# Kernel optimization log

Hardware: AMD Instinct MI355X
Metric: run time of the kernel (lower is better)

Reference implementation:

```python
import jax, jax.numpy as jnp
import numpy as np

RES = 128          # image / k-space resolution
DECIMATION = 4     # acceleration factor
P = RES * RES // DECIMATION  # 4096 trajectory points
B = 8              # batch


def setup_inputs() -> dict:
    key = jax.random.key(0)
    k1, k2 = jax.random.split(key)
    k_space_input = jax.random.normal(k1, (B, 1, RES, RES, 2), dtype=jnp.float32)
    # learnable k-space trajectory in pixel units, range [-RES/2, RES/2]
    trajectory = (jax.random.uniform(k2, (P, 2), dtype=jnp.float32) - 0.5) * RES
    return {"k_space_input": k_space_input, "trajectory": trajectory}


def _grid_sample_points(img, pts_norm):
    """torch.nn.functional.grid_sample (bilinear, zero padding, align_corners=False)
    evaluated at a list of points.
    img: (B, C, H, W); pts_norm: (P, 2) in [-1, 1], [:, 0] -> x (W axis), [:, 1] -> y (H axis).
    Returns (B, C, P)."""
    H, W = img.shape[-2], img.shape[-1]
    x = (pts_norm[:, 0] + 1.0) * (W * 0.5) - 0.5
    y = (pts_norm[:, 1] + 1.0) * (H * 0.5) - 0.5
    x0f = jnp.floor(x)
    y0f = jnp.floor(y)
    wx = x - x0f  # differentiable interpolation weights
    wy = y - y0f
    x0 = x0f.astype(jnp.int32)
    y0 = y0f.astype(jnp.int32)

    def tap(ix, iy, w):
        valid = ((ix >= 0) & (ix < W) & (iy >= 0) & (iy < H)).astype(img.dtype)
        ixc = jnp.clip(ix, 0, W - 1)
        iyc = jnp.clip(iy, 0, H - 1)
        return img[:, :, iyc, ixc] * (w * valid)  # (B, C, P)

    return (tap(x0, y0, (1 - wx) * (1 - wy))
            + tap(x0 + 1, y0, wx * (1 - wy))
            + tap(x0, y0 + 1, (1 - wx) * wy)
            + tap(x0 + 1, y0 + 1, wx * wy))


def _forward(k_space_input, trajectory):
    # (B,1,H,W,2) -> (B,2,H,W): channels = (real, imag)
    ksp = jnp.transpose(k_space_input, (0, 1, 4, 2, 3))[:, 0]
    # bilinear resampling of cartesian k-space at the trajectory points
    pts = trajectory / (RES * 0.5)  # normalize to [-1, 1] as in the torch helper
    sub = _grid_sample_points(ksp, pts)            # (B, 2, P)
    c = sub[:, 0] + 1j * sub[:, 1]                 # complex measurements (B, P)
    # adjoint (type-1) NUFFT back to a centered RES x RES image grid:
    # img[y, x] = (1/RES) * sum_p c[p] * exp(+2*pi*i*(ky_p*y + kx_p*x)/RES)
    xs = jnp.arange(RES, dtype=jnp.float32) - RES * 0.5  # centered grid coords
    phase = (2.0 * jnp.pi / RES)
    Ax = jnp.exp(1j * phase * trajectory[:, 0][:, None] * xs[None, :])  # (P, W)
    Ay = jnp.exp(1j * phase * trajectory[:, 1][:, None] * xs[None, :])  # (P, H)
    tmp = c[:, :, None] * Ay[None, :, :]           # (B, P, H)
    img = jnp.einsum('bph,pw->bhw', tmp, Ax) / RES  # (B, H, W), 1/sqrt(H*W) scale
    out = jnp.stack([img.real, img.imag], axis=-1)[:, None]  # (B, 1, H, W, 2)
    return out


def reference(k_space_input, trajectory):
    return _forward(k_space_input, trajectory)
```

## Files before the change

### kernel.cpp

```cpp
#include <hip/hip_runtime.h>

#define RES    128
#define P_PTS  4096
#define CHUNKS 32
#define PP     128

typedef _Float16 half8  __attribute__((ext_vector_type(8)));
typedef _Float16 half2v __attribute__((ext_vector_type(2)));
typedef float    f32x4  __attribute__((ext_vector_type(4)));

__global__ __launch_bounds__(256) void gemm_kernel(const float* __restrict__ ksp,
                                                   const float* __restrict__ traj,
                                                   half2v* __restrict__ part) {
    __shared__ float stx[PP], sty[PP];
    __shared__ float2 sc[PP];
    __shared__ __align__(16) _Float16 sA[2][4096];
    __shared__ __align__(16) _Float16 sB[2][8192];

    const int chunk = blockIdx.x;
    const int b     = blockIdx.y >> 1;
    const int mh    = blockIdx.y & 1;
    const int tid   = threadIdx.x;
    const int wave  = tid >> 6;
    const int lane  = tid & 63;
    const int l15   = lane & 15;
    const int q     = lane >> 4;

    if (tid < PP) {
        const int p = chunk * PP + tid;
        const float tx = traj[2 * p], ty = traj[2 * p + 1];
        stx[tid] = tx;
        sty[tid] = ty;
        const float x = tx + 63.5f, y = ty + 63.5f;
        const float x0f = floorf(x), y0f = floorf(y);
        const float wx = x - x0f, wy = y - y0f;
        const int ix0 = (int)x0f, iy0 = (int)y0f;
        float re = 0.0f, im = 0.0f;
#pragma unroll
        for (int dy = 0; dy < 2; ++dy) {
#pragma unroll
            for (int dx = 0; dx < 2; ++dx) {
                const int ix = ix0 + dx, iy = iy0 + dy;
                const float w = (dx ? wx : 1.0f - wx) * (dy ? wy : 1.0f - wy);
                if (ix >= 0 && ix < RES && iy >= 0 && iy < RES) {
                    const float2 v = *(const float2*)(ksp + ((b * RES + iy) * RES + ix) * 2);
                    re = fmaf(v.x, w, re);
                    im = fmaf(v.y, w, im);
                }
            }
        }
        sc[tid] = make_float2(re * (1.0f / 128.0f), im * (1.0f / 128.0f));
    }
    __syncthreads();

    f32x4 accR[4][2], accI[4][2];
#pragma unroll
    for (int i = 0; i < 4; ++i)
#pragma unroll
        for (int j = 0; j < 2; ++j) {
            accR[i][j] = (f32x4){0.f, 0.f, 0.f, 0.f};
            accI[i][j] = (f32x4){0.f, 0.f, 0.f, 0.f};
        }

    const float inv = 1.0f / 128.0f;
    const int nB = tid & 127, kB = tid >> 7;
    const int mA = tid & 63,  kA = tid >> 6;
    const float xn = ((float)nB - 64.0f) * inv;
    const float xm = ((float)(mh * 64 + mA) - 64.0f) * inv;

    for (int r = 0; r < 4; ++r) {
        const int p0  = r * 32;
        const int buf = r & 1;
#pragma unroll
        for (int i = 0; i < 4; ++i) {
            const int k8l = kB + 2 * i;
            half8 v;
#pragma unroll
            for (int j = 0; j < 4; ++j) {
                const int pl = p0 + k8l * 4 + j;
                const float rev = stx[pl] * xn;
                const float f = rev - floorf(rev);
                v[2 * j]     = (_Float16)__builtin_amdgcn_cosf(f);
                v[2 * j + 1] = (_Float16)__builtin_amdgcn_sinf(f);
            }
            *(half8*)(&sB[buf][(k8l * 128 + nB) * 8]) = v;
        }
#pragma unroll
        for (int i = 0; i < 2; ++i) {
            const int k8l = kA + 4 * i;
            half8 v;
#pragma unroll
            for (int j = 0; j < 4; ++j) {
                const int pl = p0 + k8l * 4 + j;
                const float rev = sty[pl] * xm;
                const float f = rev - floorf(rev);
                const float cs = __builtin_amdgcn_cosf(f);
                const float sn = __builtin_amdgcn_sinf(f);
                const float cr = sc[pl].x, ci = sc[pl].y;
                v[2 * j]     = (_Float16)(cr * cs - ci * sn);
                v[2 * j + 1] = (_Float16)(cr * sn + ci * cs);
            }
            *(half8*)(&sA[buf][(k8l * 64 + mA) * 8]) = v;
        }
        __syncthreads();

#pragma unroll
        for (int s = 0; s < 2; ++s) {
            const _Float16* pa = &sA[buf][(s * 4 + q) * 512];
            const _Float16* pb = &sB[buf][(s * 4 + q) * 1024];
            half8 an[4], bv[2], a1[4], a2[4];
#pragma unroll
            for (int mt = 0; mt < 4; ++mt)
                an[mt] = *(const half8*)(pa + (mt * 16 + l15) * 8);
#pragma unroll
            for (int nt = 0; nt < 2; ++nt)
                bv[nt] = *(const half8*)(pb + (wave * 32 + nt * 16 + l15) * 8);
            const half8 SGN = {(_Float16)1.f, (_Float16)-1.f, (_Float16)1.f, (_Float16)-1.f,
                               (_Float16)1.f, (_Float16)-1.f, (_Float16)1.f, (_Float16)-1.f};
#pragma unroll
            for (int mt = 0; mt < 4; ++mt) {
                a1[mt] = an[mt] * SGN;
                a2[mt] = __builtin_shufflevector(an[mt], an[mt],
                                                 1, 0, 3, 2, 5, 4, 7, 6);
            }
#pragma unroll
            for (int mt = 0; mt < 4; ++mt)
#pragma unroll
                for (int nt = 0; nt < 2; ++nt) {
                    accR[mt][nt] = __builtin_amdgcn_mfma_f32_16x16x32_f16(
                        a1[mt], bv[nt], accR[mt][nt], 0, 0, 0);
                    accI[mt][nt] = __builtin_amdgcn_mfma_f32_16x16x32_f16(
                        a2[mt], bv[nt], accI[mt][nt], 0, 0, 0);
                }
        }
    }

#pragma unroll
    for (int mt = 0; mt < 4; ++mt) {
#pragma unroll
        for (int nt = 0; nt < 2; ++nt) {
            const int n = wave * 32 + nt * 16 + l15;
#pragma unroll
            for (int rg = 0; rg < 4; ++rg) {
                const int m = b * 128 + mh * 64 + mt * 16 + q * 4 + rg;
                half2v pv;
                pv[0] = (_Float16)accR[mt][nt][rg];
                pv[1] = (_Float16)accI[mt][nt][rg];
                part[(size_t)chunk * 131072 + m * 128 + n] = pv;
            }
        }
    }
}

__global__ __launch_bounds__(256) void reduce_kernel(const half2v* __restrict__ part,
                                                     float2* __restrict__ out) {
    const int i = blockIdx.x * 256 + threadIdx.x;
    float sr = 0.f, si = 0.f;
#pragma unroll
    for (int c = 0; c < CHUNKS; ++c) {
        half2v v = part[(size_t)c * 131072 + i];
        sr += (float)v[0];
        si += (float)v[1];
    }
    out[i] = make_float2(sr, si);
}

extern "C" void kernel_launch(void* const* d_in, const int* in_sizes, int n_in,
                              void* d_out, int out_size, void* d_ws, size_t ws_size,
                              hipStream_t stream) {
    const float* ksp  = (const float*)d_in[0];
    const float* traj = (const float*)d_in[1];
    half2v* part = (half2v*)d_ws;

    hipLaunchKernelGGL(gemm_kernel,   dim3(CHUNKS, 16), dim3(256), 0, stream,
                       ksp, traj, part);
    hipLaunchKernelGGL(reduce_kernel, dim3(512),        dim3(256), 0, stream,
                       part, (float2*)d_out);
}
```

Before: 75.49 us.

## Fuse GEMM and reduction into one cooperative kernel with grid sync

Merges the partial-sum GEMM kernel and the chunk reduction kernel into a single cooperative launch, separated by a threadfence and a grid-wide barrier. This removes one kernel launch and the inter-kernel gap. It also replaces floor-based fractional reduction with the fract intrinsic and interleaves A-fragment loads with the MFMAs to lower register pressure. In exchange, cooperative launch adds grid-sync overhead and requires all 512 blocks to be co-resident.

Result: slower. 198.9 us (+163.4%).

```diff
diff --git a/kernel.cpp b/kernel.cpp
--- a/kernel.cpp
+++ b/kernel.cpp
@@ -1,4 +1,7 @@
 #include <hip/hip_runtime.h>
+#include <hip/hip_cooperative_groups.h>
+
+namespace cg = cooperative_groups;
 
 #define RES    128
 #define P_PTS  4096
@@ -9,9 +12,10 @@
 typedef _Float16 half2v __attribute__((ext_vector_type(2)));
 typedef float    f32x4  __attribute__((ext_vector_type(4)));
 
-__global__ __launch_bounds__(256) void gemm_kernel(const float* __restrict__ ksp,
-                                                   const float* __restrict__ traj,
-                                                   half2v* __restrict__ part) {
+__global__ __launch_bounds__(256) void fused_kernel(const float* __restrict__ ksp,
+                                                    const float* __restrict__ traj,
+                                                    half2v* __restrict__ part,
+                                                    float2* __restrict__ out) {
     __shared__ float stx[PP], sty[PP];
     __shared__ float2 sc[PP];
     __shared__ __align__(16) _Float16 sA[2][4096];
@@ -78,8 +82,7 @@
 #pragma unroll
             for (int j = 0; j < 4; ++j) {
                 const int pl = p0 + k8l * 4 + j;
-                const float rev = stx[pl] * xn;
-                const float f = rev - floorf(rev);
+                const float f = __builtin_amdgcn_fractf(stx[pl] * xn);
                 v[2 * j]     = (_Float16)__builtin_amdgcn_cosf(f);
                 v[2 * j + 1] = (_Float16)__builtin_amdgcn_sinf(f);
             }
@@ -92,8 +95,7 @@
 #pragma unroll
             for (int j = 0; j < 4; ++j) {
                 const int pl = p0 + k8l * 4 + j;
-                const float rev = sty[pl] * xm;
-                const float f = rev - floorf(rev);
+                const float f = __builtin_amdgcn_fractf(sty[pl] * xm);
                 const float cs = __builtin_amdgcn_cosf(f);
                 const float sn = __builtin_amdgcn_sinf(f);
                 const float cr = sc[pl].x, ci = sc[pl].y;
@@ -108,10 +110,7 @@
         for (int s = 0; s < 2; ++s) {
             const _Float16* pa = &sA[buf][(s * 4 + q) * 512];
             const _Float16* pb = &sB[buf][(s * 4 + q) * 1024];
-            half8 an[4], bv[2], a1[4], a2[4];
-#pragma unroll
-            for (int mt = 0; mt < 4; ++mt)
-                an[mt] = *(const half8*)(pa + (mt * 16 + l15) * 8);
+            half8 bv[2];
 #pragma unroll
             for (int nt = 0; nt < 2; ++nt)
                 bv[nt] = *(const half8*)(pb + (wave * 32 + nt * 16 + l15) * 8);
@@ -119,19 +118,18 @@
                                (_Float16)1.f, (_Float16)-1.f, (_Float16)1.f, (_Float16)-1.f};
 #pragma unroll
             for (int mt = 0; mt < 4; ++mt) {
-                a1[mt] = an[mt] * SGN;
-                a2[mt] = __builtin_shufflevector(an[mt], an[mt],
+                const half8 an = *(const half8*)(pa + (mt * 16 + l15) * 8);
+                const half8 a1 = an * SGN;
+                const half8 a2 = __builtin_shufflevector(an, an,
                                                  1, 0, 3, 2, 5, 4, 7, 6);
-            }
-#pragma unroll
-            for (int mt = 0; mt < 4; ++mt)
 #pragma unroll
                 for (int nt = 0; nt < 2; ++nt) {
                     accR[mt][nt] = __builtin_amdgcn_mfma_f32_16x16x32_f16(
-                        a1[mt], bv[nt], accR[mt][nt], 0, 0, 0);
+                        a1, bv[nt], accR[mt][nt], 0, 0, 0);
                     accI[mt][nt] = __builtin_amdgcn_mfma_f32_16x16x32_f16(
-                        a2[mt], bv[nt], accI[mt][nt], 0, 0, 0);
+                        a2, bv[nt], accI[mt][nt], 0, 0, 0);
                 }
+            }
         }
     }
 
@@ -150,11 +148,11 @@
             }
         }
     }
-}
 
-__global__ __launch_bounds__(256) void reduce_kernel(const half2v* __restrict__ part,
-                                                     float2* __restrict__ out) {
-    const int i = blockIdx.x * 256 + threadIdx.x;
+    __threadfence();
+    cg::this_grid().sync();
+
+    const int i = (blockIdx.y * 32 + blockIdx.x) * 256 + tid;
     float sr = 0.f, si = 0.f;
 #pragma unroll
     for (int c = 0; c < CHUNKS; ++c) {
@@ -171,9 +169,9 @@
     const float* ksp  = (const float*)d_in[0];
     const float* traj = (const float*)d_in[1];
     half2v* part = (half2v*)d_ws;
+    float2* out  = (float2*)d_out;
 
-    hipLaunchKernelGGL(gemm_kernel,   dim3(CHUNKS, 16), dim3(256), 0, stream,
-                       ksp, traj, part);
-    hipLaunchKernelGGL(reduce_kernel, dim3(512),        dim3(256), 0, stream,
-                       part, (float2*)d_out);
+    void* args[] = { (void*)&ksp, (void*)&traj, (void*)&part, (void*)&out };
+    hipLaunchCooperativeKernel((const void*)fused_kernel,
+                               dim3(CHUNKS, 16), dim3(256), args, 0, stream);
 }
```

## Generate MFMA operands in registers via rotation recurrence, drop LDS staging

Applied to the files above, without the earlier changes.

Each wave now builds its A and B MFMA fragments directly in registers instead of staging twiddle tiles through double-buffered shared memory with barriers. Per-point rotation factors (exp(2πi·t·16/128)) are precomputed once, so the phases for the other m and n tiles come from complex multiplications rather than extra sin/cos calls. This removes LDS writes, LDS reads and the per-round __syncthreads, and cuts transcendental count. In exchange each wave redundantly computes the twiddles, and the chained rotations add some fp error.

Result: no change. 75.17 us (-0.4%).

```diff
diff --git a/kernel.cpp b/kernel.cpp
--- a/kernel.cpp
+++ b/kernel.cpp
@@ -4,6 +4,7 @@
 #define P_PTS  4096
 #define CHUNKS 32
 #define PP     128
+#define STEPS  8
 
 typedef _Float16 half8  __attribute__((ext_vector_type(8)));
 typedef _Float16 half2v __attribute__((ext_vector_type(2)));
@@ -12,10 +13,8 @@
 __global__ __launch_bounds__(256) void gemm_kernel(const float* __restrict__ ksp,
                                                    const float* __restrict__ traj,
                                                    half2v* __restrict__ part) {
-    __shared__ float stx[PP], sty[PP];
-    __shared__ float2 sc[PP];
-    __shared__ __align__(16) _Float16 sA[2][4096];
-    __shared__ __align__(16) _Float16 sB[2][8192];
+    __shared__ float4 sP1[PP];
+    __shared__ float4 sP2[PP];
 
     const int chunk = blockIdx.x;
     const int b     = blockIdx.y >> 1;
@@ -29,8 +28,6 @@
     if (tid < PP) {
         const int p = chunk * PP + tid;
         const float tx = traj[2 * p], ty = traj[2 * p + 1];
-        stx[tid] = tx;
-        sty[tid] = ty;
         const float x = tx + 63.5f, y = ty + 63.5f;
         const float x0f = floorf(x), y0f = floorf(y);
         const float wx = x - x0f, wy = y - y0f;
@@ -49,7 +46,12 @@
                 }
             }
         }
-        sc[tid] = make_float2(re * (1.0f / 128.0f), im * (1.0f / 128.0f));
+        const float fx = __builtin_amdgcn_fractf(tx * 0.125f);
+        const float fy = __builtin_amdgcn_fractf(ty * 0.125f);
+        sP1[tid] = make_float4(tx, ty,
+                               __builtin_amdgcn_cosf(fx), __builtin_amdgcn_sinf(fx));
+        sP2[tid] = make_float4(re * (1.0f / 128.0f), im * (1.0f / 128.0f),
+                               __builtin_amdgcn_cosf(fy), __builtin_amdgcn_sinf(fy));
     }
     __syncthreads();
 
@@ -63,76 +65,57 @@
         }
 
     const float inv = 1.0f / 128.0f;
-    const int nB = tid & 127, kB = tid >> 7;
-    const int mA = tid & 63,  kA = tid >> 6;
-    const float xn = ((float)nB - 64.0f) * inv;
-    const float xm = ((float)(mh * 64 + mA) - 64.0f) * inv;
+    const float xm0 = ((float)(mh * 64 + l15) - 64.0f) * inv;
+    const float xn0 = ((float)(wave * 32 + l15) - 64.0f) * inv;
 
-    for (int r = 0; r < 4; ++r) {
-        const int p0  = r * 32;
-        const int buf = r & 1;
+    for (int s = 0; s < STEPS; ++s) {
+        half8 a1[4], a2[4], bv[2];
+        float4 P1v[4], P2v[4];
 #pragma unroll
-        for (int i = 0; i < 4; ++i) {
-            const int k8l = kB + 2 * i;
-            half8 v;
-#pragma unroll
-            for (int j = 0; j < 4; ++j) {
-                const int pl = p0 + k8l * 4 + j;
-                const float rev = stx[pl] * xn;
-                const float f = rev - floorf(rev);
-                v[2 * j]     = (_Float16)__builtin_amdgcn_cosf(f);
-                v[2 * j + 1] = (_Float16)__builtin_amdgcn_sinf(f);
-            }
-            *(half8*)(&sB[buf][(k8l * 128 + nB) * 8]) = v;
+        for (int jj = 0; jj < 4; ++jj) {
+            const int pl = s * 16 + q * 4 + jj;
+            P1v[jj] = sP1[pl];
+            P2v[jj] = sP2[pl];
         }
 #pragma unroll
-        for (int i = 0; i < 2; ++i) {
-            const int k8l = kA + 4 * i;
-            half8 v;
-#pragma unroll
-            for (int j = 0; j < 4; ++j) {
-                const int pl = p0 + k8l * 4 + j;
-                const float rev = sty[pl] * xm;
-                const float f = rev - floorf(rev);
-                const float cs = __builtin_amdgcn_cosf(f);
-                const float sn = __builtin_amdgcn_sinf(f);
-                const float cr = sc[pl].x, ci = sc[pl].y;
-                v[2 * j]     = (_Float16)(cr * cs - ci * sn);
-                v[2 * j + 1] = (_Float16)(cr * sn + ci * cs);
-            }
-            *(half8*)(&sA[buf][(k8l * 64 + mA) * 8]) = v;
-        }
-        __syncthreads();
-
-#pragma unroll
-        for (int s = 0; s < 2; ++s) {
-            const _Float16* pa = &sA[buf][(s * 4 + q) * 512];
-            const _Float16* pb = &sB[buf][(s * 4 + q) * 1024];
-            half8 an[4], bv[2], a1[4], a2[4];
-#pragma unroll
-            for (int mt = 0; mt < 4; ++mt)
-                an[mt] = *(const half8*)(pa + (mt * 16 + l15) * 8);
-#pragma unroll
-            for (int nt = 0; nt < 2; ++nt)
-                bv[nt] = *(const half8*)(pb + (wave * 32 + nt * 16 + l15) * 8);
-            const half8 SGN = {(_Float16)1.f, (_Float16)-1.f, (_Float16)1.f, (_Float16)-1.f,
-                               (_Float16)1.f, (_Float16)-1.f, (_Float16)1.f, (_Float16)-1.f};
+        for (int jj = 0; jj < 4; ++jj) {
+            const float4 P1 = P1v[jj], P2 = P2v[jj];
+            const float fb = __builtin_amdgcn_fractf(P1.x * xn0);
+            const float bc = __builtin_amdgcn_cosf(fb);
+            const float bs = __builtin_amdgcn_sinf(fb);
+            bv[0][2 * jj]     = (_Float16)bc;
+            bv[0][2 * jj + 1] = (_Float16)bs;
+            const float bc1 = bc * P1.z - bs * P1.w;
+            const float bs1 = bc * P1.w + bs * P1.z;
+            bv[1][2 * jj]     = (_Float16)bc1;
+            bv[1][2 * jj + 1] = (_Float16)bs1;
+            const float fa = __builtin_amdgcn_fractf(P1.y * xm0);
+            const float ac = __builtin_amdgcn_cosf(fa);
+            const float as = __builtin_amdgcn_sinf(fa);
+            float ar = P2.x * ac - P2.y * as;
+            float ai = P2.x * as + P2.y * ac;
 #pragma unroll
             for (int mt = 0; mt < 4; ++mt) {
-                a1[mt] = an[mt] * SGN;
-                a2[mt] = __builtin_shufflevector(an[mt], an[mt],
-                                                 1, 0, 3, 2, 5, 4, 7, 6);
+                a1[mt][2 * jj]     = (_Float16)ar;
+                a1[mt][2 * jj + 1] = (_Float16)(-ai);
+                a2[mt][2 * jj]     = (_Float16)ai;
+                a2[mt][2 * jj + 1] = (_Float16)ar;
+                if (mt < 3) {
+                    const float nr = ar * P2.z - ai * P2.w;
+                    const float ni = ar * P2.w + ai * P2.z;
+                    ar = nr; ai = ni;
+                }
             }
+        }
 #pragma unroll
-            for (int mt = 0; mt < 4; ++mt)
+        for (int mt = 0; mt < 4; ++mt)
 #pragma unroll
-                for (int nt = 0; nt < 2; ++nt) {
-                    accR[mt][nt] = __builtin_amdgcn_mfma_f32_16x16x32_f16(
-                        a1[mt], bv[nt], accR[mt][nt], 0, 0, 0);
-                    accI[mt][nt] = __builtin_amdgcn_mfma_f32_16x16x32_f16(
-                        a2[mt], bv[nt], accI[mt][nt], 0, 0, 0);
-                }
-        }
+            for (int nt = 0; nt < 2; ++nt) {
+                accR[mt][nt] = __builtin_amdgcn_mfma_f32_16x16x32_f16(
+                    a1[mt], bv[nt], accR[mt][nt], 0, 0, 0);
+                accI[mt][nt] = __builtin_amdgcn_mfma_f32_16x16x32_f16(
+                    a2[mt], bv[nt], accI[mt][nt], 0, 0, 0);
+            }
     }
 
 #pragma unroll
```
